# Performance work log

Hardware: AMD Instinct MI355X
Metric: run time of the kernel (lower is better)

The kernel has to match this reference:

```python
import jax, jax.numpy as jnp
import numpy as np

IN_DIM, H1, H2, N_CLASSES = 128, 100, 128, 19
BATCH, SEQ = 512, 256


def _lstm_relu(x, W, U, b, units):
    """Keras LSTM with activation='relu', recurrent_activation='sigmoid'.
    x: [B, T, D]. Returns (all hidden states [B, T, units], last hidden [B, units]).
    Gate order (Keras): i, f, g(cell candidate), o.
    """
    B = x.shape[0]
    h0 = jnp.zeros((B, units), x.dtype)
    c0 = jnp.zeros((B, units), x.dtype)

    # precompute input projections for all timesteps: [T, B, 4*units]
    zx = jnp.einsum('btd,dk->tbk', x, W) + b

    def step(carry, zx_t):
        h, c = carry
        z = zx_t + h @ U
        i, f, g, o = jnp.split(z, 4, axis=-1)
        i = jax.nn.sigmoid(i)
        f = jax.nn.sigmoid(f)
        g = jax.nn.relu(g)          # activation='relu'
        o = jax.nn.sigmoid(o)
        c = f * c + i * g
        h = o * jax.nn.relu(c)      # output activation is also relu
        return (h, c), h

    (h_last, _), hs = jax.lax.scan(step, (h0, c0), zx)
    return jnp.transpose(hs, (1, 0, 2)), h_last


def setup_inputs() -> dict:
    key = jax.random.key(0)
    ks = jax.random.split(key, 9)
    def w(k, shape, fan_in):
        return jax.random.normal(k, shape, jnp.float32) / np.sqrt(fan_in)
    x = jax.random.normal(ks[0], (BATCH, SEQ, IN_DIM), jnp.float32)
    return {
        'x': x,
        'W1': w(ks[1], (IN_DIM, 4 * H1), IN_DIM),
        'U1': w(ks[2], (H1, 4 * H1), H1),
        'b1': jnp.zeros((4 * H1,), jnp.float32),
        'W2': w(ks[3], (H1, 4 * H2), H1),
        'U2': w(ks[4], (H2, 4 * H2), H2),
        'b2': jnp.zeros((4 * H2,), jnp.float32),
        'Wd': w(ks[5], (H2, N_CLASSES), H2),
        'bd': jnp.zeros((N_CLASSES,), jnp.float32),
    }


def reference(x, W1, U1, b1, W2, U2, b2, Wd, bd):
    h1_seq, _ = _lstm_relu(x, W1, U1, b1, H1)      # [B, T, 100]
    _, h2 = _lstm_relu(h1_seq, W2, U2, b2, H2)     # [B, 128] (last step only)
    logits = h2 @ Wd + bd
    return jax.nn.softmax(logits, axis=-1)         # [B, 19]
```

## Files before the change

### kernel.cpp

```cpp
#include <hip/hip_runtime.h>
#include <math.h>


#define T_SEQ 256
#define BATCH 512
#define IN_DIM 128
#define H1 100
#define H2 128
#define NCLS 19

typedef float f4v __attribute__((ext_vector_type(4)));

__device__ __forceinline__ float sigmoidf_(float x) {
    return 1.0f / (1.0f + __expf(-x));
}
__device__ __forceinline__ float hsum4_(f4v v) {
    return (v.x + v.y) + (v.z + v.w);
}

#define REP8(M)  M(0) M(1) M(2) M(3) M(4) M(5) M(6) M(7)
#define REP25(M) M(0) M(1) M(2) M(3) M(4) M(5) M(6) M(7) M(8) M(9) M(10) M(11) \
                 M(12) M(13) M(14) M(15) M(16) M(17) M(18) M(19) M(20) M(21) M(22) M(23) M(24)

template<int K, int N, bool SWAP>
__global__ __launch_bounds__(256, 2)
void proj_kernel(const float* __restrict__ A, const float* __restrict__ W,
                 const float* __restrict__ bias, float* __restrict__ out)
{
    constexpr int LDA = 132;
    constexpr int WCG = 260;
    __shared__ __align__(16) float As[32 * LDA];
    __shared__ __align__(16) float Ws[16 * WCG];
    const int tid = threadIdx.x;
    const int r0 = blockIdx.x * 128;
    const int c0 = blockIdx.y * 128;
    const int ty = tid >> 4, tx = tid & 15;

#define PACC(i) f4v accL##i = {0.f,0.f,0.f,0.f}; f4v accR##i = {0.f,0.f,0.f,0.f};
    REP8(PACC)
#undef PACC

    for (int kk = 0; kk < K; kk += 32) {
        __syncthreads();
#pragma unroll
        for (int i = 0; i < 4; ++i) {
            int idx = tid + i * 256;
            int row = idx >> 3, kg = idx & 7;
            int k = kk + kg * 4;
            f4v v = {0.f, 0.f, 0.f, 0.f};
            if (k < K) v = *(const f4v*)&A[(size_t)(r0 + row) * K + k];
            As[(kg * 4 + 0) * LDA + row] = v.x;
            As[(kg * 4 + 1) * LDA + row] = v.y;
            As[(kg * 4 + 2) * LDA + row] = v.z;
            As[(kg * 4 + 3) * LDA + row] = v.w;
        }
#pragma unroll
        for (int i = 0; i < 4; ++i) {
            int idx = tid + i * 256;
            int k = idx >> 5, q = idx & 31;
            int gk = kk + k, gc = c0 + q * 4;
            f4v v = {0.f, 0.f, 0.f, 0.f};
            if (gk < K && gc < N) v = *(const f4v*)&W[(size_t)gk * N + gc];
            int cg = q >> 1, half = q & 1;
            *(f4v*)&Ws[cg * WCG + k * 8 + half * 4] = v;
        }
        __syncthreads();
#pragma unroll
        for (int k = 0; k < 32; ++k) {
            f4v av0 = *(const f4v*)&As[k * LDA + ty * 8];
            f4v av1 = *(const f4v*)&As[k * LDA + ty * 8 + 4];
            f4v b0v = *(const f4v*)&Ws[tx * WCG + k * 8];
            f4v b1v = *(const f4v*)&Ws[tx * WCG + k * 8 + 4];
#define PFMA(i, s) accL##i += (s) * b0v; accR##i += (s) * b1v;
            PFMA(0, av0.x) PFMA(1, av0.y) PFMA(2, av0.z) PFMA(3, av0.w)
            PFMA(4, av1.x) PFMA(5, av1.y) PFMA(6, av1.z) PFMA(7, av1.w)
#undef PFMA
        }
    }

    const int cb = c0 + tx * 8;
    float b0 = (cb + 0 < N) ? bias[cb + 0] : 0.f;
    float b1 = (cb + 1 < N) ? bias[cb + 1] : 0.f;
    float b2 = (cb + 2 < N) ? bias[cb + 2] : 0.f;
    float b3 = (cb + 3 < N) ? bias[cb + 3] : 0.f;
    float b4 = (cb + 4 < N) ? bias[cb + 4] : 0.f;
    float b5 = (cb + 5 < N) ? bias[cb + 5] : 0.f;
    float b6 = (cb + 6 < N) ? bias[cb + 6] : 0.f;
    float b7 = (cb + 7 < N) ? bias[cb + 7] : 0.f;
    f4v bL = {b0, b1, b2, b3};
    f4v bR = {b4, b5, b6, b7};
#define PST(i) { \
        int r = r0 + ty * 8 + i; \
        size_t orow = SWAP ? ((size_t)(r & 255) * BATCH + (r >> 8)) : (size_t)r; \
        if (cb < N)     { f4v v = accL##i + bL; *(f4v*)&out[orow * N + cb] = v; } \
        if (cb + 4 < N) { f4v v = accR##i + bR; *(f4v*)&out[orow * N + cb + 4] = v; } }
    REP8(PST)
#undef PST
}

__global__ __launch_bounds__(256)
__attribute__((amdgpu_waves_per_eu(1, 1)))
void rec1_kernel(const float* __restrict__ zx,
                 const float* __restrict__ U1,
                 float* __restrict__ h1seq)
{
    const int row = blockIdx.x;
    const int tid = threadIdx.x;
    const int g = tid >> 6;
    const int l = tid & 63;
    const bool has2 = (l < 36);
    const int u0 = l;
    const int u1 = 64 + (has2 ? l : 35);
    const int c0 = g * 100 + u0;
    const int c1 = g * 100 + u1;
    __shared__ __align__(16) float hs[104];
    __shared__ float ga[3][104];

#define W_LD(j) \
    f4v wa_##j, wb_##j; { \
        const float* p = U1 + (size_t)(4 * (j)) * 400; \
        wa_##j = (f4v){p[c0], p[400 + c0], p[800 + c0], p[1200 + c0]}; \
        wb_##j = (f4v){p[c1], p[400 + c1], p[800 + c1], p[1200 + c1]}; }
    REP25(W_LD)
#undef W_LD

    if (tid < 104) hs[tid] = 0.0f;
    float cs0 = 0.0f, cs1 = 0.0f;
    const float* pz0 = zx + (size_t)row * 400;
    float zc0 = pz0[c0];
    float zc1 = pz0[c1];
    __syncthreads();

    for (int t = 0; t < T_SEQ; ++t) {
        int tn = (t + 1 < T_SEQ) ? t + 1 : t;
        const float* pz = zx + ((size_t)tn * BATCH + row) * 400;
        float zn0 = pz[c0];
        float zn1 = pz[c1];

        f4v s0 = {0.f, 0.f, 0.f, 0.f};
        f4v s1 = {0.f, 0.f, 0.f, 0.f};
#define W_F(j) { f4v hv = *(const f4v*)&hs[4 * (j)]; s0 += hv * wa_##j; s1 += hv * wb_##j; }
        REP25(W_F)
#undef W_F
        float a0 = zc0 + hsum4_(s0);
        float a1 = zc1 + hsum4_(s1);
        if (g == 2) { a0 = fmaxf(a0, 0.0f); a1 = fmaxf(a1, 0.0f); }
        else        { a0 = sigmoidf_(a0);   a1 = sigmoidf_(a1);   }
        if (g != 0) {
            ga[g - 1][u0] = a0;
            if (has2) ga[g - 1][u1] = a1;
        }
        __syncthreads();

        if (g == 0) {
            float f0 = ga[0][u0], q0 = ga[1][u0], o0 = ga[2][u0];
            cs0 = f0 * cs0 + a0 * q0;
            float h0 = o0 * fmaxf(cs0, 0.0f);
            hs[u0] = h0;
            float* ph = h1seq + ((size_t)t * BATCH + row) * H1;
            ph[u0] = h0;
            if (has2) {
                float f1 = ga[0][u1], q1 = ga[1][u1], o1 = ga[2][u1];
                cs1 = f1 * cs1 + a1 * q1;
                float h1v = o1 * fmaxf(cs1, 0.0f);
                hs[u1] = h1v;
                ph[u1] = h1v;
            }
        }
        __syncthreads();
        zc0 = zn0;
        zc1 = zn1;
    }
}

template<bool INIT, bool LAST>
__global__ __launch_bounds__(512)
__attribute__((amdgpu_waves_per_eu(2, 2)))
void rec2_chunk(const float* __restrict__ zx,
                const float* __restrict__ U2,
                float* __restrict__ cbuf,
                float* __restrict__ hbuf,
                float* __restrict__ h2out,
                int tlen)
{
    const int row = blockIdx.x;
    const int tid = threadIdx.x;
    const int kq = tid >> 7;
    const int cl = tid & 127;
    __shared__ __align__(16) float hs[H2];
    __shared__ float zp[4 * 512];
    __shared__ float za[512];

#define R2_LD(j) \
    f4v w0_##j, w1_##j, w2_##j, w3_##j; { \
        const float* p = U2 + (size_t)(kq * 32 + 4 * j) * 512 + cl; \
        w0_##j = (f4v){p[0],   p[512],       p[1024],       p[1536]}; \
        w1_##j = (f4v){p[128], p[512 + 128], p[1024 + 128], p[1536 + 128]}; \
        w2_##j = (f4v){p[256], p[512 + 256], p[1024 + 256], p[1536 + 256]}; \
        w3_##j = (f4v){p[384], p[512 + 384], p[1024 + 384], p[1536 + 384]}; }
    REP8(R2_LD)
#undef R2_LD
#define R2P(j) asm volatile("" : "+v"(w0_##j), "+v"(w1_##j), "+v"(w2_##j), "+v"(w3_##j));
    REP8(R2P)
#undef R2P

    float cst = 0.0f;
    if (tid < H2) {
        if (INIT) {
            hs[tid] = 0.0f;
        } else {
            hs[tid] = hbuf[(size_t)row * H2 + tid];
            cst = cbuf[(size_t)row * H2 + tid];
        }
    }
    float zc = zx[(size_t)row * 512 + tid];
    __syncthreads();

    for (int t = 0; t < tlen; ++t) {
        int tn = (t + 1 < tlen) ? t + 1 : t;
        float zn = zx[((size_t)tn * BATCH + row) * 512 + tid];

        f4v s0 = {0.f, 0.f, 0.f, 0.f};
        f4v s1 = {0.f, 0.f, 0.f, 0.f};
        f4v s2 = {0.f, 0.f, 0.f, 0.f};
        f4v s3 = {0.f, 0.f, 0.f, 0.f};
#define R2_FMA(j) { f4v hv = *(const f4v*)&hs[kq * 32 + 4 * j]; \
        s0 += hv * w0_##j; s1 += hv * w1_##j; s2 += hv * w2_##j; s3 += hv * w3_##j; }
        REP8(R2_FMA)
#undef R2_FMA
        zp[kq * 512 + cl]       = hsum4_(s0);
        zp[kq * 512 + cl + 128] = hsum4_(s1);
        zp[kq * 512 + cl + 256] = hsum4_(s2);
        zp[kq * 512 + cl + 384] = hsum4_(s3);
        __syncthreads();

        float z = zc + (zp[tid] + zp[512 + tid]) + (zp[1024 + tid] + zp[1536 + tid]);
        float a = (tid >= 2 * H2 && tid < 3 * H2) ? fmaxf(z, 0.0f) : sigmoidf_(z);
        za[tid] = a;
        __syncthreads();

        if (tid < H2) {
            float i = za[tid], f = za[tid + 128], g = za[tid + 256], o = za[tid + 384];
            cst = f * cst + i * g;
            hs[tid] = o * fmaxf(cst, 0.0f);
        }
        __syncthreads();
        zc = zn;
    }

    if (tid < H2) {
        float h = hs[tid];
        cbuf[(size_t)row * H2 + tid] = cst;
        hbuf[(size_t)row * H2 + tid] = h;
        if (LAST) h2out[(size_t)row * H2 + tid] = h;
    }
}

__global__ __launch_bounds__(64, 1)
void dense_softmax_kernel(const float* __restrict__ h2, const float* __restrict__ Wd,
                          const float* __restrict__ bd, float* __restrict__ out)
{
    const int b = blockIdx.x;
    const int k = threadIdx.x;
    __shared__ __align__(16) float hsm[H2];
    if (k < H2 / 4) ((f4v*)hsm)[k] = ((const f4v*)(h2 + (size_t)b * H2))[k];
    __syncthreads();

    float logit = -1e30f;
    if (k < NCLS) {
        float acc = bd[k];
#pragma unroll
        for (int d = 0; d < H2; ++d) acc += hsm[d] * Wd[d * NCLS + k];
        logit = acc;
    }
    float m = logit;
#pragma unroll
    for (int off = 32; off >= 1; off >>= 1) m = fmaxf(m, __shfl_xor(m, off, 64));
    float e = (k < NCLS) ? __expf(logit - m) : 0.0f;
    float s = e;
#pragma unroll
    for (int off = 32; off >= 1; off >>= 1) s += __shfl_xor(s, off, 64);
    if (k < NCLS) out[(size_t)b * NCLS + k] = e / s;
}

__global__ __launch_bounds__(448, 1)
void lstm1_fb(const float* __restrict__ x, const float* __restrict__ W1,
              const float* __restrict__ U1, const float* __restrict__ b1,
              float* __restrict__ h1out)
{
    const int b = blockIdx.x;
    const int k = threadIdx.x;
    __shared__ __align__(16) float xs[IN_DIM];
    __shared__ __align__(16) float hs[H1];
    __shared__ __align__(16) float zs[4 * H1];
    float w1r[IN_DIM];
    float u1r[H1];
    float bias = 0.0f;
    if (k < 4 * H1) {
        bias = b1[k];
#pragma unroll
        for (int d = 0; d < IN_DIM; ++d) w1r[d] = W1[d * (4 * H1) + k];
#pragma unroll
        for (int j = 0; j < H1; ++j) u1r[j] = U1[j * (4 * H1) + k];
    }
    if (k < H1) hs[k] = 0.0f;
    if (k < IN_DIM / 4)
        ((float4*)xs)[k] = ((const float4*)(x + ((size_t)b * T_SEQ) * IN_DIM))[k];
    float c = 0.0f;
    __syncthreads();
    for (int t = 0; t < T_SEQ; ++t) {
        if (k < 4 * H1) {
            float acc0 = bias, acc1 = 0.f, acc2 = 0.f, acc3 = 0.f;
#pragma unroll
            for (int q = 0; q < IN_DIM / 4; ++q) {
                float4 xv = ((const float4*)xs)[q];
                acc0 += xv.x * w1r[4 * q]; acc1 += xv.y * w1r[4 * q + 1];
                acc2 += xv.z * w1r[4 * q + 2]; acc3 += xv.w * w1r[4 * q + 3];
            }
#pragma unroll
            for (int q = 0; q < H1 / 4; ++q) {
                float4 hv = ((const float4*)hs)[q];
                acc0 += hv.x * u1r[4 * q]; acc1 += hv.y * u1r[4 * q + 1];
                acc2 += hv.z * u1r[4 * q + 2]; acc3 += hv.w * u1r[4 * q + 3];
            }
            float zv = (acc0 + acc1) + (acc2 + acc3);
            zs[k] = (k >= 2 * H1 && k < 3 * H1) ? fmaxf(zv, 0.0f) : sigmoidf_(zv);
        }
        __syncthreads();
        if (k < H1) {
            float i = zs[k], f = zs[k + H1], g = zs[k + 2 * H1], o = zs[k + 3 * H1];
            c = f * c + i * g;
            float h = o * fmaxf(c, 0.0f);
            hs[k] = h;
            h1out[((size_t)t * BATCH + b) * H1 + k] = h;
        }
        int tn = t + 1;
        if (tn < T_SEQ && k < IN_DIM / 4)
            ((float4*)xs)[k] = ((const float4*)(x + ((size_t)b * T_SEQ + tn) * IN_DIM))[k];
        __syncthreads();
    }
}

__global__ __launch_bounds__(512, 1)
void lstm2_fb(const float* __restrict__ h1in, const float* __restrict__ W2,
              const float* __restrict__ U2, const float* __restrict__ b2,
              float* __restrict__ h2out)
{
    const int b = blockIdx.x;
    const int k = threadIdx.x;
    __shared__ __align__(16) float ps[H1];
    __shared__ __align__(16) float hs[H2];
    __shared__ __align__(16) float zs[4 * H2];
    float w2r[H1];
    float u2r[H2];
    float bias = b2[k];
#pragma unroll
    for (int j = 0; j < H1; ++j) w2r[j] = W2[j * (4 * H2) + k];
#pragma unroll
    for (int j = 0; j < H2; ++j) u2r[j] = U2[j * (4 * H2) + k];
    if (k < H2) hs[k] = 0.0f;
    if (k < H1 / 4)
        ((float4*)ps)[k] = ((const float4*)(h1in + (size_t)b * H1))[k];
    float c = 0.0f;
    float hlast = 0.0f;
    __syncthreads();
    for (int t = 0; t < T_SEQ; ++t) {
        float acc0 = bias, acc1 = 0.f, acc2 = 0.f, acc3 = 0.f;
#pragma unroll
        for (int q = 0; q < H1 / 4; ++q) {
            float4 pv = ((const float4*)ps)[q];
            acc0 += pv.x * w2r[4 * q]; acc1 += pv.y * w2r[4 * q + 1];
            acc2 += pv.z * w2r[4 * q + 2]; acc3 += pv.w * w2r[4 * q + 3];
        }
#pragma unroll
        for (int q = 0; q < H2 / 4; ++q) {
            float4 hv = ((const float4*)hs)[q];
            acc0 += hv.x * u2r[4 * q]; acc1 += hv.y * u2r[4 * q + 1];
            acc2 += hv.z * u2r[4 * q + 2]; acc3 += hv.w * u2r[4 * q + 3];
        }
        float zv = (acc0 + acc1) + (acc2 + acc3);
        zs[k] = (k >= 2 * H2 && k < 3 * H2) ? fmaxf(zv, 0.0f) : sigmoidf_(zv);
        __syncthreads();
        if (k < H2) {
            float i = zs[k], f = zs[k + H2], g = zs[k + 2 * H2], o = zs[k + 3 * H2];
            c = f * c + i * g;
            hlast = o * fmaxf(c, 0.0f);
            hs[k] = hlast;
        }
        int tn = t + 1;
        if (tn < T_SEQ && k < H1 / 4)
            ((float4*)ps)[k] = ((const float4*)(h1in + ((size_t)tn * BATCH + b) * H1))[k];
        __syncthreads();
    }
    if (k < H2) h2out[(size_t)b * H2 + k] = hlast;
}

extern "C" void kernel_launch(void* const* d_in, const int* in_sizes, int n_in,
                              void* d_out, int out_size, void* d_ws, size_t ws_size,
                              hipStream_t stream) {
    const float* x  = (const float*)d_in[0];
    const float* W1 = (const float*)d_in[1];
    const float* U1 = (const float*)d_in[2];
    const float* b1 = (const float*)d_in[3];
    const float* W2 = (const float*)d_in[4];
    const float* U2 = (const float*)d_in[5];
    const float* b2 = (const float*)d_in[6];
    const float* Wd = (const float*)d_in[7];
    const float* bd = (const float*)d_in[8];
    float* out = (float*)d_out;

    const size_t zx_elems = (size_t)T_SEQ * BATCH * 400;
    const size_t h1_elems = (size_t)T_SEQ * BATCH * H1;
    const size_t st_elems = (size_t)BATCH * H2;
    const size_t need = (zx_elems + h1_elems + 3 * st_elems) * sizeof(float);

    if (ws_size >= need) {
        float* zxbuf = (float*)d_ws;
        float* h1buf = zxbuf + zx_elems;
        float* cbuf  = h1buf + h1_elems;
        float* hbuf  = cbuf + st_elems;
        float* h2buf = hbuf + st_elems;
        const int TC = T_SEQ / 2;

        hipLaunchKernelGGL((proj_kernel<IN_DIM, 4 * H1, true>), dim3(1024, 4), dim3(256), 0, stream,
                           x, W1, b1, zxbuf);
        hipLaunchKernelGGL(rec1_kernel, dim3(BATCH), dim3(256), 0, stream,
                           zxbuf, U1, h1buf);
        hipLaunchKernelGGL((proj_kernel<H1, 4 * H2, false>), dim3(512, 4), dim3(256), 0, stream,
                           h1buf, W2, b2, zxbuf);
        hipLaunchKernelGGL((rec2_chunk<true, false>), dim3(BATCH), dim3(512), 0, stream,
                           zxbuf, U2, cbuf, hbuf, h2buf, TC);
        hipLaunchKernelGGL((proj_kernel<H1, 4 * H2, false>), dim3(512, 4), dim3(256), 0, stream,
                           h1buf + (size_t)TC * BATCH * H1, W2, b2, zxbuf);
        hipLaunchKernelGGL((rec2_chunk<false, true>), dim3(BATCH), dim3(512), 0, stream,
                           zxbuf, U2, cbuf, hbuf, h2buf, TC);

        hipLaunchKernelGGL(dense_softmax_kernel, dim3(BATCH), dim3(64), 0, stream,
                           h2buf, Wd, bd, out);
    } else {
        float* h1buf = (float*)d_ws;
        float* h2buf = h1buf + h1_elems;
        hipLaunchKernelGGL(lstm1_fb, dim3(BATCH), dim3(448), 0, stream, x, W1, U1, b1, h1buf);
        hipLaunchKernelGGL(lstm2_fb, dim3(BATCH), dim3(512), 0, stream, h1buf, W2, U2, b2, h2buf);
        hipLaunchKernelGGL(dense_softmax_kernel, dim3(BATCH), dim3(64), 0, stream, h2buf, Wd, bd, out);
    }
}
```

Before: 1.309 ms.

## Move layer-1 recurrent weights to LDS and process two batch rows per block

The first-layer recurrence now stages all of U1 in about 160KB of dynamic LDS instead of keeping slices in registers. Each 512-thread block handles two batch rows, so 256 blocks fill the GPU in a single wave instead of two. Each thread computes all four gates for one hidden unit over half the K range and combines the halves with a lane shuffle. A double-buffered h array cuts the step to one barrier instead of two. The trade-off is that every step rereads the weights from LDS, with possible bank conflicts, in place of register-resident operands.

```diff
diff --git a/kernel.cpp b/kernel.cpp
--- a/kernel.cpp
+++ b/kernel.cpp
@@ -19,8 +19,7 @@
 }
 
 #define REP8(M)  M(0) M(1) M(2) M(3) M(4) M(5) M(6) M(7)
-#define REP25(M) M(0) M(1) M(2) M(3) M(4) M(5) M(6) M(7) M(8) M(9) M(10) M(11) \
-                 M(12) M(13) M(14) M(15) M(16) M(17) M(18) M(19) M(20) M(21) M(22) M(23) M(24)
+#define REP13(M) M(0) M(1) M(2) M(3) M(4) M(5) M(6) M(7) M(8) M(9) M(10) M(11) M(12)
 
 template<int K, int N, bool SWAP>
 __global__ __launch_bounds__(256, 2)
@@ -98,78 +97,77 @@
 #undef PST
 }
 
-__global__ __launch_bounds__(256)
-__attribute__((amdgpu_waves_per_eu(1, 1)))
+__global__ __launch_bounds__(512, 1)
 void rec1_kernel(const float* __restrict__ zx,
                  const float* __restrict__ U1,
                  float* __restrict__ h1seq)
 {
-    const int row = blockIdx.x;
+    extern __shared__ float Wl[];
+    __shared__ __align__(16) float hs2[2][2][104];
     const int tid = threadIdx.x;
-    const int g = tid >> 6;
-    const int l = tid & 63;
-    const bool has2 = (l < 36);
-    const int u0 = l;
-    const int u1 = 64 + (has2 ? l : 35);
-    const int c0 = g * 100 + u0;
-    const int c1 = g * 100 + u1;
-    __shared__ __align__(16) float hs[104];
-    __shared__ float ga[3][104];
-
-#define W_LD(j) \
-    f4v wa_##j, wb_##j; { \
-        const float* p = U1 + (size_t)(4 * (j)) * 400; \
-        wa_##j = (f4v){p[c0], p[400 + c0], p[800 + c0], p[1200 + c0]}; \
-        wb_##j = (f4v){p[c1], p[400 + c1], p[800 + c1], p[1200 + c1]}; }
-    REP25(W_LD)
-#undef W_LD
-
-    if (tid < 104) hs[tid] = 0.0f;
-    float cs0 = 0.0f, cs1 = 0.0f;
-    const float* pz0 = zx + (size_t)row * 400;
-    float zc0 = pz0[c0];
-    float zc1 = pz0[c1];
+    const int row = tid & 1;
+    const int ks  = (tid >> 1) & 1;
+    const int cl  = tid >> 2;
+    const bool act = (cl < H1);
+    const int cc  = act ? cl : 0;
+    const int brow = blockIdx.x * 2 + row;
+    const int k0 = ks * 52;
+
+    for (int k = 0; k < H1; ++k) {
+        if (tid < 400) Wl[tid * 100 + k] = U1[(size_t)k * 400 + tid];
+    }
+    {
+        float* h4 = &hs2[0][0][0];
+        if (tid < 416) h4[tid] = 0.0f;
+    }
+    const int wc0 = (0 * 100 + cc) * 100;
+    const int wc1 = (1 * 100 + cc) * 100;
+    const int wc2 = (2 * 100 + cc) * 100;
+    const int wc3 = (3 * 100 + cc) * 100;
+
+    float cst = 0.0f;
+    const float* pz0 = zx + (size_t)brow * 400 + cc;
+    float zc0 = pz0[0], zc1 = pz0[100], zc2 = pz0[200], zc3 = pz0[300];
     __syncthreads();
 
     for (int t = 0; t < T_SEQ; ++t) {
         int tn = (t + 1 < T_SEQ) ? t + 1 : t;
-        const float* pz = zx + ((size_t)tn * BATCH + row) * 400;
-        float zn0 = pz[c0];
-        float zn1 = pz[c1];
-
-        f4v s0 = {0.f, 0.f, 0.f, 0.f};
-        f4v s1 = {0.f, 0.f, 0.f, 0.f};
-#define W_F(j) { f4v hv = *(const f4v*)&hs[4 * (j)]; s0 += hv * wa_##j; s1 += hv * wb_##j; }
-        REP25(W_F)
-#undef W_F
-        float a0 = zc0 + hsum4_(s0);
-        float a1 = zc1 + hsum4_(s1);
-        if (g == 2) { a0 = fmaxf(a0, 0.0f); a1 = fmaxf(a1, 0.0f); }
-        else        { a0 = sigmoidf_(a0);   a1 = sigmoidf_(a1);   }
-        if (g != 0) {
-            ga[g - 1][u0] = a0;
-            if (has2) ga[g - 1][u1] = a1;
-        }
-        __syncthreads();
-
-        if (g == 0) {
-            float f0 = ga[0][u0], q0 = ga[1][u0], o0 = ga[2][u0];
-            cs0 = f0 * cs0 + a0 * q0;
-            float h0 = o0 * fmaxf(cs0, 0.0f);
-            hs[u0] = h0;
-            float* ph = h1seq + ((size_t)t * BATCH + row) * H1;
-            ph[u0] = h0;
-            if (has2) {
-                float f1 = ga[0][u1], q1 = ga[1][u1], o1 = ga[2][u1];
-                cs1 = f1 * cs1 + a1 * q1;
-                float h1v = o1 * fmaxf(cs1, 0.0f);
-                hs[u1] = h1v;
-                ph[u1] = h1v;
+        const float* pz = zx + ((size_t)tn * BATCH + brow) * 400 + cc;
+        float zn0 = pz[0], zn1 = pz[100], zn2 = pz[200], zn3 = pz[300];
+
+        float a0 = 0.f, a1 = 0.f, a2 = 0.f, a3 = 0.f;
+        if (act) {
+            const float* hb = &hs2[t & 1][row][0];
+            f4v s0 = {0.f,0.f,0.f,0.f};
+            f4v s1 = {0.f,0.f,0.f,0.f};
+            f4v s2 = {0.f,0.f,0.f,0.f};
+            f4v s3 = {0.f,0.f,0.f,0.f};
+#define R1F(j) { f4v hv = *(const f4v*)&hb[k0 + 4*(j)]; \
+            s0 += hv * *(const f4v*)&Wl[wc0 + k0 + 4*(j)]; \
+            s1 += hv * *(const f4v*)&Wl[wc1 + k0 + 4*(j)]; \
+            s2 += hv * *(const f4v*)&Wl[wc2 + k0 + 4*(j)]; \
+            s3 += hv * *(const f4v*)&Wl[wc3 + k0 + 4*(j)]; }
+            REP13(R1F)
+#undef R1F
+            a0 = hsum4_(s0); a1 = hsum4_(s1); a2 = hsum4_(s2); a3 = hsum4_(s3);
+            a0 += __shfl_xor(a0, 2, 64);
+            a1 += __shfl_xor(a1, 2, 64);
+            a2 += __shfl_xor(a2, 2, 64);
+            a3 += __shfl_xor(a3, 2, 64);
+
+            float iv = sigmoidf_(zc0 + a0);
+            float fv = sigmoidf_(zc1 + a1);
+            float gv = fmaxf(zc2 + a2, 0.0f);
+            float ov = sigmoidf_(zc3 + a3);
+            cst = fv * cst + iv * gv;
+            float h = ov * fmaxf(cst, 0.0f);
+            if (ks == 0) {
+                hs2[(t + 1) & 1][row][cl] = h;
+                h1seq[((size_t)t * BATCH + brow) * H1 + cl] = h;
             }
         }
         __syncthreads();
-        zc0 = zn0;
-        zc1 = zn1;
+        zc0 = zn0; zc1 = zn1; zc2 = zn2; zc3 = zn3;
     }
 }
 
@@ -424,7 +422,7 @@
 
         hipLaunchKernelGGL((proj_kernel<IN_DIM, 4 * H1, true>), dim3(1024, 4), dim3(256), 0, stream,
                            x, W1, b1, zxbuf);
-        hipLaunchKernelGGL(rec1_kernel, dim3(BATCH), dim3(256), 0, stream,
+        hipLaunchKernelGGL(rec1_kernel, dim3(BATCH / 2), dim3(512), 40004 * sizeof(float), stream,
                            zxbuf, U1, h1buf);
         hipLaunchKernelGGL((proj_kernel<H1, 4 * H2, false>), dim3(512, 4), dim3(256), 0, stream,
                            h1buf, W2, b2, zxbuf);
```

Measured after the change: 1.634 ms. +24.8%, slower.
